# Kernel tuning notes

Measured on AMD Instinct MI355X. Metric: run time of the kernel, lower is better.

## Reference

```python
import jax, jax.numpy as jnp
import numpy as np

FS = 16            # fixStride
LAST_RATIO = 0.5
TAUA, TAUB = 10.0, 0.1
TOT_EPOCHS = 100
EPS = 1e-20
SEED = 777


def _safe_norm(diff):
    # ||diff||_2 with subgradient 0 at 0 (matches torch.norm backward at 0)
    sq = jnp.sum(diff * diff, axis=-1)
    d = jnp.sqrt(jnp.where(sq > 0, sq, 1.0))
    return jnp.where(sq > 0, d, 0.0)


def _forward(x, w_score, b_score, att_params, num_graphs, epoch):
    BN, C = x.shape
    B = int(num_graphs)
    N = BN // B
    RES = N - FS + 1                       # rows per graph (unfold1d)
    MAXP = int(np.ceil(N * LAST_RATIO))    # max_pivot_count = ceil(N*last_ratio/init_ratio)

    # --- TopKPool scorer (init_ratio==1.0): permute nodes per graph by desc score
    scores = (x @ w_score + b_score) / jnp.sqrt(jnp.sum(w_score ** 2))
    perm = jnp.argsort(-scores.reshape(B, N), axis=-1, stable=True)      # [B,N]
    xg = jnp.take_along_axis(x.reshape(B, N, C), perm[..., None], axis=1)

    # --- sliding-window edges: row r -> dests r..r+FS-1, src node r
    dst = jnp.arange(RES)[:, None] + jnp.arange(FS)[None, :]             # [RES,FS]
    x_src = xg[:, :RES, :]                                               # [B,RES,C]
    x_dst = xg[:, dst, :]                                                # [B,RES,FS,C]

    # getSM_ei + scatter_softmax over rows: att = [x_s, x_d] @ att_params
    a1, a2 = att_params[:C], att_params[C:]
    sm = jax.nn.softmax((xg @ a1)[:, :RES, None] + (xg @ a2)[:, dst], axis=-1)  # [B,RES,FS]

    # getDM_ei (sigma=1): gaussian-kernel edge distances
    gk = jnp.exp(-_safe_norm(x_src[:, :, None, :] - x_dst) / 2.0) - EPS  # [B,RES,FS]

    # scatterSort: stable descending sort of gk per row
    order = jnp.argsort(-gk, axis=-1, stable=True)
    gk_sort = jnp.take_along_axis(gk, order, axis=-1)
    sm_sort = jnp.take_along_axis(sm, order, axis=-1)

    # per-rank column logits: scatter-sum of sorted attention over rows of each graph
    logits = jnp.broadcast_to(sm_sort.sum(axis=1)[:, None, :], (B, RES, FS))
    logits = logits.at[:, :, 0].set(-jnp.inf)            # mask rank-0 (self edge)

    # gumbel-softmax with annealed temperature
    tau0 = TAUA * (TAUB / TAUA) ** (float(epoch) / TOT_EPOCHS)
    g = jax.random.gumbel(jax.random.key(SEED), (B, RES, FS), jnp.float32)
    gmb = jax.nn.softmax((g + logits) / tau0, axis=-1)

    # per-row threshold and shifted distances (unsorted layout)
    ths = jnp.sum(gk_sort * gmb, axis=-1, keepdims=True)
    shifted = jax.nn.relu(gk - ths)                      # [B,RES,FS]

    # scatter_min over positions 1..FS-1 (position 0 excluded via index redirect)
    delta = (jnp.argmin(shifted[:, :, 1:], axis=-1) + 1).astype(jnp.int32)  # [B,RES]

    # innerLoopStar: follow skip pointers from row 0, up to MAXP pivots
    def chain(delta_g):
        def step(ptr, _):
            valid = ptr < RES
            piv = jnp.where(valid, ptr, -1)
            nxt = jnp.where(valid, ptr + delta_g[jnp.clip(ptr, 0, RES - 1)], jnp.int32(RES))
            return nxt, piv
        _, pivs = jax.lax.scan(step, jnp.int32(0), None, length=MAXP)
        return pivs

    pivots = jax.vmap(chain)(delta)                      # [B,MAXP], -1 padded
    mask = pivots >= 0
    pooled = jnp.take_along_axis(xg, jnp.clip(pivots, 0, N - 1)[..., None], axis=1)
    pooled = pooled * mask[..., None]                    # [B,MAXP,C]
    return pooled, shifted, pivots


def setup_inputs() -> dict:
    key = jax.random.key(0)
    k0, k1, k2, k3 = jax.random.split(key, 4)
    B, N, C = 128, 512, 64
    return {
        "x": jax.random.normal(k0, (B * N, C), jnp.float32),
        "w_score": jax.random.normal(k1, (C,), jnp.float32),
        "b_score": jax.random.normal(k2, (), jnp.float32),
        "att_params": jax.random.normal(k3, (2 * C,), jnp.float32),
        "num_graphs": B,
        "epoch": 10,
    }


def reference(x, w_score, b_score, att_params, num_graphs, epoch):
    return _forward(x, w_score, b_score, att_params, num_graphs, epoch)
```

## Files before the change

kernel.cpp:

```cpp
#include <hip/hip_runtime.h>
#include <math.h>

#define BB 128
#define NN 512
#define CC 64
#define FS 16
#define RES 497
#define MAXP 256
#define BN (BB*NN)
#define GT (BB*RES*FS)
#define WPB 16
#define NCH 32
#define ROWS (WPB+FS-1)
#define PITCH 66

__device__ __forceinline__ unsigned rotl32(unsigned x, int d){ return (x<<d)|(x>>(32-d)); }

__device__ __forceinline__ void threefry777(unsigned x0, unsigned x1, unsigned &o0, unsigned &o1){
  const unsigned ks0 = 0u, ks1 = 777u;
  const unsigned ks2 = 0x1BD11BDAu ^ ks0 ^ ks1;
  x0 += ks0; x1 += ks1;
  x0+=x1; x1=rotl32(x1,13); x1^=x0;
  x0+=x1; x1=rotl32(x1,15); x1^=x0;
  x0+=x1; x1=rotl32(x1,26); x1^=x0;
  x0+=x1; x1=rotl32(x1, 6); x1^=x0;
  x0+=ks1; x1+=ks2+1u;
  x0+=x1; x1=rotl32(x1,17); x1^=x0;
  x0+=x1; x1=rotl32(x1,29); x1^=x0;
  x0+=x1; x1=rotl32(x1,16); x1^=x0;
  x0+=x1; x1=rotl32(x1,24); x1^=x0;
  x0+=ks2; x1+=ks0+2u;
  x0+=x1; x1=rotl32(x1,13); x1^=x0;
  x0+=x1; x1=rotl32(x1,15); x1^=x0;
  x0+=x1; x1=rotl32(x1,26); x1^=x0;
  x0+=x1; x1=rotl32(x1, 6); x1^=x0;
  x0+=ks0; x1+=ks1+3u;
  x0+=x1; x1=rotl32(x1,17); x1^=x0;
  x0+=x1; x1=rotl32(x1,29); x1^=x0;
  x0+=x1; x1=rotl32(x1,16); x1^=x0;
  x0+=x1; x1=rotl32(x1,24); x1^=x0;
  x0+=ks1; x1+=ks2+4u;
  x0+=x1; x1=rotl32(x1,13); x1^=x0;
  x0+=x1; x1=rotl32(x1,15); x1^=x0;
  x0+=x1; x1=rotl32(x1,26); x1^=x0;
  x0+=x1; x1=rotl32(x1, 6); x1^=x0;
  x0+=ks2; x1+=ks0+5u;
  o0 = x0; o1 = x1;
}

__device__ __forceinline__ float gumbel_at_f32(unsigned p){
  unsigned o0, o1;
  threefry777(0u, p, o0, o1);
  unsigned bits = o0 ^ o1;
  float fl = __uint_as_float((bits >> 9) | 0x3f800000u) - 1.0f;
  float u  = fmaxf(1.17549435e-38f, fl);
  return -logf(-logf(u));
}

__device__ __forceinline__ double wave_push_f64(double v, int dstLane){
  int lo = __double2loint(v), hi = __double2hiint(v);
  int plo = __builtin_amdgcn_ds_permute(dstLane<<2, lo);
  int phi = __builtin_amdgcn_ds_permute(dstLane<<2, hi);
  return __hiloint2double(phi, plo);
}

__global__ __launch_bounds__(NN) void k_scoresort(const float* __restrict__ x,
    const float* __restrict__ w, const float* __restrict__ bsc,
    const float* __restrict__ att, double* __restrict__ s1s,
    double* __restrict__ s2s, int* __restrict__ perm){
  int b = blockIdx.x, t = threadIdx.x;
  __shared__ double ss[NN];
  __shared__ int    si[NN];
  __shared__ double l1[NN], l2[NN];

  double wn=0.0, dw=0.0, d1=0.0, d2=0.0;
  #pragma unroll
  for (int c=0;c<CC;c++){ double wv=(double)w[c]; wn += wv*wv; }
  const float4* xr = (const float4*)(x + (size_t)(b*NN+t)*CC);
  #pragma unroll
  for (int q=0;q<CC/4;q++){
    float4 v = xr[q];
    double xv;
    xv=(double)v.x; dw+=xv*(double)w[4*q+0]; d1+=xv*(double)att[4*q+0]; d2+=xv*(double)att[CC+4*q+0];
    xv=(double)v.y; dw+=xv*(double)w[4*q+1]; d1+=xv*(double)att[4*q+1]; d2+=xv*(double)att[CC+4*q+1];
    xv=(double)v.z; dw+=xv*(double)w[4*q+2]; d1+=xv*(double)att[4*q+2]; d2+=xv*(double)att[CC+4*q+2];
    xv=(double)v.w; dw+=xv*(double)w[4*q+3]; d1+=xv*(double)att[4*q+3]; d2+=xv*(double)att[CC+4*q+3];
  }
  double s = (dw + (double)bsc[0]) / sqrt(wn);
  int idx = t;
  l1[t] = d1;
  l2[t] = d2;

  for (int k = 2; k <= NN; k <<= 1){
    bool up = ((t & k) == 0);
    for (int j = k >> 1; j >= 64; j >>= 1){
      ss[t] = s; si[t] = idx;
      __syncthreads();
      double os = ss[t ^ j]; int oi = si[t ^ j];
      bool first = ((t & j) == 0);
      bool cmp = (s > os) || (s == os && idx < oi);
      bool keep = (cmp == (first == up));
      if (!keep){ s = os; idx = oi; }
      __syncthreads();
    }
    #pragma unroll
    for (int j = 32; j > 0; j >>= 1){
      if (j <= (k >> 1)){
        double os = __shfl_xor(s, j, 64);
        int    oi = __shfl_xor(idx, j, 64);
        bool first = ((t & j) == 0);
        bool cmp = (s > os) || (s == os && idx < oi);
        bool keep = (cmp == (first == up));
        if (!keep){ s = os; idx = oi; }
      }
    }
  }
  __syncthreads();
  perm[b*NN + t] = idx;
  s1s[b*NN + t] = l1[idx];
  s2s[b*NN + t] = l2[idx];
}

__global__ __launch_bounds__(256) void k_passA(const float* __restrict__ x,
    const int* __restrict__ perm, const double* __restrict__ s1s,
    const double* __restrict__ s2s, double* __restrict__ gkd,
    unsigned char* __restrict__ rank8, double* __restrict__ partial){
  int b = blockIdx.y, ch = blockIdx.x, tid = threadIdx.x;
  int i0 = ch*WPB;
  int nwin  = min(WPB, RES - i0);
  int nrows = min(ROWS, NN - i0);
  __shared__ float  xs[ROWS*PITCH];
  __shared__ int    pg[ROWS];
  __shared__ double wred[4][FS];

  if (tid < nrows) pg[tid] = perm[b*NN + i0 + tid];
  __syncthreads();
  for (int u = tid; u < nrows*16; u += 256){
    int r = u >> 4, seg = u & 15;
    float4 v = ((const float4*)(x + (size_t)(b*NN + pg[r])*CC))[seg];
    float2* dst = (float2*)&xs[r*PITCH + seg*4];
    dst[0] = make_float2(v.x, v.y);
    dst[1] = make_float2(v.z, v.w);
  }
  __syncthreads();

  int w = tid >> 4, j = tid & 15;
  int lane = tid & 63, gbase = lane & 48, wv = tid >> 6;
  bool act = (w < nwin);
  int i = i0 + w;

  double sq = 0.0;
  const float* rs = &xs[w*PITCH];
  const float* rd = &xs[(w+j)*PITCH];
  #pragma unroll
  for (int c2=0;c2<CC/2;c2++){
    float2 a  = *(const float2*)&rs[2*c2];
    float2 bb = *(const float2*)&rd[2*c2];
    double d0 = (double)a.x - (double)bb.x;
    double d1v= (double)a.y - (double)bb.y;
    sq += d0*d0;
    sq += d1v*d1v;
  }
  double d   = (sq > 0.0) ? sqrt(sq) : 0.0;
  double gkv = exp(-d*0.5) - 1e-20;

  int drow = min(i + j, NN-1);
  double smt = s1s[b*NN + i] + s2s[b*NN + drow];
  double m = smt;
  #pragma unroll
  for (int off=8; off; off>>=1) m = fmax(m, __shfl_xor(m, off, 16));
  double em = exp(smt - m);
  double ssum = em;
  #pragma unroll
  for (int off=8; off; off>>=1) ssum += __shfl_xor(ssum, off, 16);
  double smn = em / ssum;

  int rank = 0;
  #pragma unroll
  for (int k=0;k<16;k++){
    double gkk = __shfl(gkv, gbase + k, 64);
    rank += ((gkk > gkv) || (gkk == gkv && k < j)) ? 1 : 0;
  }

  if (act){
    size_t base = ((size_t)b*RES + i)*FS;
    gkd[base + j]   = gkv;
    rank8[base + j] = (unsigned char)rank;
  }

  double contrib = act ? smn : 0.0;
  double srt = wave_push_f64(contrib, gbase + rank);
  srt += __shfl_xor(srt, 16, 64);
  srt += __shfl_xor(srt, 32, 64);
  if (lane < FS) wred[wv][lane] = srt;
  __syncthreads();
  if (tid < FS){
    partial[((size_t)b*NCH + ch)*FS + tid] =
        wred[0][tid] + wred[1][tid] + wred[2][tid] + wred[3][tid];
  }
}

__global__ __launch_bounds__(1024) void k_tail(const double* __restrict__ gkd,
    const unsigned char* __restrict__ rank8, const double* __restrict__ partial,
    const int* __restrict__ epoch_p, const int* __restrict__ perm,
    const float* __restrict__ x, float* __restrict__ shifted_out,
    float* __restrict__ piv_out, float* __restrict__ pooled){
  int b = blockIdx.x, tid = threadIdx.x;
  __shared__ double pl[NCH*FS];
  __shared__ double cs[FS];
  __shared__ int    tbl[8][512];
  __shared__ int    pivS[MAXP];

  if (tid < NCH*FS) pl[tid] = partial[(size_t)b*NCH*FS + tid];
  for (int i2 = tid; i2 < 512; i2 += 1024) if (i2 >= RES) tbl[0][i2] = RES;
  __syncthreads();
  if (tid < FS){
    double a = 0.0;
    #pragma unroll
    for (int ch=0; ch<NCH; ch++) a += pl[ch*FS + tid];
    cs[tid] = a;
  }
  __syncthreads();

  double tau = 10.0 * pow(0.01, (double)epoch_p[0] / 100.0);
  int lane = tid & 63, gbase = lane & 48;
  int s = tid & 15;

  #pragma unroll
  for (int it=0; it<8; it++){
    int win = it*64 + (tid >> 4);
    if (win < RES){
      size_t base = ((size_t)b*RES + win)*FS;
      double z;
      if (s == 0) z = -(double)INFINITY;
      else {
        double g = (double)gumbel_at_f32((unsigned)(base + (unsigned)s));
        z = (g + cs[s]) / tau;
      }
      double m = z;
      #pragma unroll
      for (int off=8; off; off>>=1) m = fmax(m, __shfl_xor(m, off, 16));
      double e = (s == 0) ? 0.0 : exp(z - m);
      double ssum = e;
      #pragma unroll
      for (int off=8; off; off>>=1) ssum += __shfl_xor(ssum, off, 16);
      double gmb = e / ssum;

      double gkv = gkd[base + s];
      int rk = rank8[base + s];
      double gmbr = __shfl(gmb, gbase + rk, 64);
      double ths = gkv * gmbr;
      #pragma unroll
      for (int off=8; off; off>>=1) ths += __shfl_xor(ths, off, 16);

      double shv = fmax(gkv - ths, 0.0);
      shifted_out[base + s] = (float)shv;

      double av = (s == 0) ? (double)INFINITY : shv;
      int ai = s;
      #pragma unroll
      for (int off=8; off; off>>=1){
        double ov = __shfl_xor(av, off, 16);
        int    oi = __shfl_xor(ai, off, 16);
        if (ov < av || (ov == av && oi < ai)){ av = ov; ai = oi; }
      }
      if (s == 0){
        int v = win + ai;
        tbl[0][win] = (v > RES) ? RES : v;
      }
    }
  }
  __syncthreads();

  #pragma unroll
  for (int k=1;k<8;k++){
    if (tid < 512){ int v = tbl[k-1][tid]; tbl[k][tid] = tbl[k-1][v]; }
    __syncthreads();
  }
  if (tid < MAXP){
    int p = 0;
    #pragma unroll
    for (int k=0;k<8;k++) if ((tid>>k)&1) p = tbl[k][p];
    int piv = (p < RES) ? p : -1;
    pivS[tid] = piv;
    piv_out[b*MAXP + tid] = (float)piv;
  }
  __syncthreads();

  for (int u = tid; u < MAXP*16; u += 1024){
    int bp = u >> 4, seg = u & 15;
    int piv = pivS[bp];
    float4 v = make_float4(0.f,0.f,0.f,0.f);
    if (piv >= 0){
      int src = perm[b*NN + piv];
      v = ((const float4*)(x + (size_t)(b*NN + src)*CC))[seg];
    }
    ((float4*)pooled)[(size_t)(b*MAXP + bp)*16 + seg] = v;
  }
}

extern "C" void kernel_launch(void* const* d_in, const int* in_sizes, int n_in,
                              void* d_out, int out_size, void* d_ws, size_t ws_size,
                              hipStream_t stream) {
  (void)in_sizes; (void)n_in; (void)out_size; (void)ws_size;
  const float* x    = (const float*)d_in[0];
  const float* w    = (const float*)d_in[1];
  const float* bsc  = (const float*)d_in[2];
  const float* att  = (const float*)d_in[3];
  const int*   epch = (const int*)d_in[5];

  double* s1s     = (double*)d_ws;
  double* s2s     = s1s + BN;
  double* gkd     = s2s + BN;
  double* partial = gkd + GT;
  int*    perm    = (int*)(partial + (size_t)BB*NCH*FS);
  unsigned char* rank8 = (unsigned char*)(perm + BN);

  float* out_pooled  = (float*)d_out;
  float* out_shifted = out_pooled + BB*MAXP*CC;
  float* out_piv     = out_shifted + (size_t)BB*RES*FS;

  k_scoresort<<<BB, NN, 0, stream>>>(x, w, bsc, att, s1s, s2s, perm);
  k_passA <<<dim3(NCH, BB), 256, 0, stream>>>(x, perm, s1s, s2s, gkd, rank8, partial);
  k_tail  <<<BB, 1024, 0, stream>>>(gkd, rank8, partial, epch, perm, x,
                                    out_shifted, out_piv, out_pooled);
}
```

Measured before the change: 66.39 us.

## Split tail kernel into parallel gumbel pass and pointer-chain pooling kernel

The single per-graph tail kernel (128 blocks of 1024 threads looping over 8 window chunks) is split into k_gumbel, launched with 8×128 blocks that each handle 64 windows and write per-row argmin offsets to a workspace delta buffer, and k_chainpool, which builds the pointer-doubling table from delta and gathers pooled rows with 256 threads per graph. This raises parallelism for the FP64-heavy gumbel softmax stage, which previously ran on only 128 blocks. The cost is an extra kernel launch, a global round trip for delta, and each gumbel block redundantly reducing the partial column sums.

```diff
diff --git a/kernel.cpp b/kernel.cpp
--- a/kernel.cpp
+++ b/kernel.cpp
@@ -13,6 +13,8 @@
 #define NCH 32
 #define ROWS (WPB+FS-1)
 #define PITCH 66
+#define GWIN 64
+#define GBLK 8
 
 __device__ __forceinline__ unsigned rotl32(unsigned x, int d){ return (x<<d)|(x>>(32-d)); }
 
@@ -200,19 +202,18 @@
   }
 }
 
-__global__ __launch_bounds__(1024) void k_tail(const double* __restrict__ gkd,
+__global__ __launch_bounds__(1024) void k_gumbel(const double* __restrict__ gkd,
     const unsigned char* __restrict__ rank8, const double* __restrict__ partial,
-    const int* __restrict__ epoch_p, const int* __restrict__ perm,
-    const float* __restrict__ x, float* __restrict__ shifted_out,
-    float* __restrict__ piv_out, float* __restrict__ pooled){
-  int b = blockIdx.x, tid = threadIdx.x;
+    const int* __restrict__ epoch_p, float* __restrict__ shifted_out,
+    int* __restrict__ delta){
+  int b = blockIdx.y, tid = threadIdx.x;
+  int win = blockIdx.x*GWIN + (tid >> 4);
+  int s = tid & 15;
+  int lane = tid & 63, gbase = lane & 48;
   __shared__ double pl[NCH*FS];
   __shared__ double cs[FS];
-  __shared__ int    tbl[8][512];
-  __shared__ int    pivS[MAXP];
 
   if (tid < NCH*FS) pl[tid] = partial[(size_t)b*NCH*FS + tid];
-  for (int i2 = tid; i2 < 512; i2 += 1024) if (i2 >= RES) tbl[0][i2] = RES;
   __syncthreads();
   if (tid < FS){
     double a = 0.0;
@@ -222,62 +223,69 @@
   }
   __syncthreads();
 
+  if (win >= RES) return;
   double tau = 10.0 * pow(0.01, (double)epoch_p[0] / 100.0);
-  int lane = tid & 63, gbase = lane & 48;
-  int s = tid & 15;
-
-  #pragma unroll
-  for (int it=0; it<8; it++){
-    int win = it*64 + (tid >> 4);
-    if (win < RES){
-      size_t base = ((size_t)b*RES + win)*FS;
-      double z;
-      if (s == 0) z = -(double)INFINITY;
-      else {
-        double g = (double)gumbel_at_f32((unsigned)(base + (unsigned)s));
-        z = (g + cs[s]) / tau;
-      }
-      double m = z;
-      #pragma unroll
-      for (int off=8; off; off>>=1) m = fmax(m, __shfl_xor(m, off, 16));
-      double e = (s == 0) ? 0.0 : exp(z - m);
-      double ssum = e;
-      #pragma unroll
-      for (int off=8; off; off>>=1) ssum += __shfl_xor(ssum, off, 16);
-      double gmb = e / ssum;
-
-      double gkv = gkd[base + s];
-      int rk = rank8[base + s];
-      double gmbr = __shfl(gmb, gbase + rk, 64);
-      double ths = gkv * gmbr;
-      #pragma unroll
-      for (int off=8; off; off>>=1) ths += __shfl_xor(ths, off, 16);
-
-      double shv = fmax(gkv - ths, 0.0);
-      shifted_out[base + s] = (float)shv;
-
-      double av = (s == 0) ? (double)INFINITY : shv;
-      int ai = s;
-      #pragma unroll
-      for (int off=8; off; off>>=1){
-        double ov = __shfl_xor(av, off, 16);
-        int    oi = __shfl_xor(ai, off, 16);
-        if (ov < av || (ov == av && oi < ai)){ av = ov; ai = oi; }
-      }
-      if (s == 0){
-        int v = win + ai;
-        tbl[0][win] = (v > RES) ? RES : v;
-      }
-    }
-  }
-  __syncthreads();
-
+  size_t base = ((size_t)b*RES + win)*FS;
+
+  double z;
+  if (s == 0) z = -(double)INFINITY;
+  else {
+    double g = (double)gumbel_at_f32((unsigned)(base + (unsigned)s));
+    z = (g + cs[s]) / tau;
+  }
+  double m = z;
+  #pragma unroll
+  for (int off=8; off; off>>=1) m = fmax(m, __shfl_xor(m, off, 16));
+  double e = (s == 0) ? 0.0 : exp(z - m);
+  double ssum = e;
+  #pragma unroll
+  for (int off=8; off; off>>=1) ssum += __shfl_xor(ssum, off, 16);
+  double gmb = e / ssum;
+
+  double gkv = gkd[base + s];
+  int rk = rank8[base + s];
+  double gmbr = __shfl(gmb, gbase + rk, 64);
+  double ths = gkv * gmbr;
+  #pragma unroll
+  for (int off=8; off; off>>=1) ths += __shfl_xor(ths, off, 16);
+
+  double shv = fmax(gkv - ths, 0.0);
+  shifted_out[base + s] = (float)shv;
+
+  double av = (s == 0) ? (double)INFINITY : shv;
+  int ai = s;
+  #pragma unroll
+  for (int off=8; off; off>>=1){
+    double ov = __shfl_xor(av, off, 16);
+    int    oi = __shfl_xor(ai, off, 16);
+    if (ov < av || (ov == av && oi < ai)){ av = ov; ai = oi; }
+  }
+  if (s == 0) delta[b*RES + win] = ai;
+}
+
+__global__ __launch_bounds__(256) void k_chainpool(const int* __restrict__ delta,
+    const int* __restrict__ perm, const float* __restrict__ x,
+    float* __restrict__ piv_out, float* __restrict__ pooled){
+  int b = blockIdx.x, tid = threadIdx.x;
+  __shared__ int tbl[8][512];
+  __shared__ int pivS[MAXP];
+
+  for (int i = tid; i < 512; i += 256){
+    int v;
+    if (i < RES){ v = i + delta[b*RES + i]; if (v > RES) v = RES; }
+    else v = RES;
+    tbl[0][i] = v;
+  }
+  __syncthreads();
   #pragma unroll
   for (int k=1;k<8;k++){
-    if (tid < 512){ int v = tbl[k-1][tid]; tbl[k][tid] = tbl[k-1][v]; }
+    int v0 = tbl[k-1][tid];
+    int v1 = tbl[k-1][tid+256];
+    tbl[k][tid]     = tbl[k-1][v0];
+    tbl[k][tid+256] = tbl[k-1][v1];
     __syncthreads();
   }
-  if (tid < MAXP){
+  {
     int p = 0;
     #pragma unroll
     for (int k=0;k<8;k++) if ((tid>>k)&1) p = tbl[k][p];
@@ -287,7 +295,7 @@
   }
   __syncthreads();
 
-  for (int u = tid; u < MAXP*16; u += 1024){
+  for (int u = tid; u < MAXP*16; u += 256){
     int bp = u >> 4, seg = u & 15;
     int piv = pivS[bp];
     float4 v = make_float4(0.f,0.f,0.f,0.f);
@@ -314,14 +322,15 @@
   double* gkd     = s2s + BN;
   double* partial = gkd + GT;
   int*    perm    = (int*)(partial + (size_t)BB*NCH*FS);
-  unsigned char* rank8 = (unsigned char*)(perm + BN);
+  int*    delta   = perm + BN;
+  unsigned char* rank8 = (unsigned char*)(delta + BB*RES);
 
   float* out_pooled  = (float*)d_out;
   float* out_shifted = out_pooled + BB*MAXP*CC;
   float* out_piv     = out_shifted + (size_t)BB*RES*FS;
 
   k_scoresort<<<BB, NN, 0, stream>>>(x, w, bsc, att, s1s, s2s, perm);
-  k_passA <<<dim3(NCH, BB), 256, 0, stream>>>(x, perm, s1s, s2s, gkd, rank8, partial);
-  k_tail  <<<BB, 1024, 0, stream>>>(gkd, rank8, partial, epch, perm, x,
-                                    out_shifted, out_piv, out_pooled);
-}
+  k_passA    <<<dim3(NCH, BB), 256, 0, stream>>>(x, perm, s1s, s2s, gkd, rank8, partial);
+  k_gumbel   <<<dim3(GBLK, BB), 1024, 0, stream>>>(gkd, rank8, partial, epch, out_shifted, delta);
+  k_chainpool<<<BB, 256, 0, stream>>>(delta, perm, x, out_piv, out_pooled);
+}
```

Result: slower. 68.86 us (+3.7%).
